# Performance work log

Hardware: AMD Instinct MI355X
Metric: run time of the kernel (lower is better)

## Reference

```python
import jax, jax.numpy as jnp
import numpy as np

B, N, P, K, D = 8, 2048, 64, 32, 384
DEPTH, DI, DS, DCONV, DTR, NC = 12, 768, 16, 4, 24, 40
BN_EPS = 1e-5


def _spread_bits(v):
    v = v & 1023
    v = (v | (v << 16)) & 50331903
    v = (v | (v << 8)) & 50393103
    v = (v | (v << 4)) & 51130563
    v = (v | (v << 2)) & 153391689
    return v


def _zkey(x, y, z):
    return _spread_bits(x) | (_spread_bits(y) << 1) | (_spread_bits(z) << 2)


def _sfc_order(xyz, trans):
    lo = xyz.min(0, keepdims=True)
    hi = xyz.max(0, keepdims=True)
    q = jnp.clip(((xyz - lo) / (hi - lo + 1e-6) * 1023.0).astype(jnp.int32), 0, 1023)
    if trans:
        keys = _zkey(q[:, 2], q[:, 1], q[:, 0])
    else:
        keys = _zkey(q[:, 0], q[:, 1], q[:, 2])
    return jnp.argsort(keys)


def _ln(x, g, b):
    m = x.mean(-1, keepdims=True)
    v = jnp.var(x, axis=-1, keepdims=True)
    return (x - m) / jnp.sqrt(v + 1e-5) * g + b


def _bn_eval(x, g, b):
    # BatchNorm in eval mode, running_mean=0 / running_var=1
    return x * (g / np.float32(np.sqrt(1.0 + BN_EPS))) + b


def _patch_embed_one(xyz, w1, b1, g1, be1, w2, b2, g2, be2, w3, b3, g3, be3):
    # xyz: (N,3)
    cidx = (jnp.arange(P) * (N / P)).astype(jnp.int32)
    centers = xyz[cidx]                                      # (P,3)
    d2 = ((centers[:, None, :] - xyz[None, :, :]) ** 2).sum(-1)  # (P,N)
    _, knn = jax.lax.top_k(-d2, K)                           # (P,K) smallest dists
    nx = xyz[knn] - centers[:, None, :]                      # (P,K,3)
    h = jax.nn.gelu(_bn_eval(nx @ w1.T + b1, g1, be1), approximate=False)   # (P,K,64)
    h = jax.nn.gelu(_bn_eval(h @ w2.T + b2, g2, be2), approximate=False)    # (P,K,128)
    h = _bn_eval(h @ w3.T + b3, g3, be3)                     # (P,K,384)
    return h.max(1), centers


def _mamba(x, in_w, conv_w, conv_b, xp_w, dt_w, dt_b, Alog, Dp, out_w):
    # x: (B,L,D)
    Bsz, L, _ = x.shape
    xz = x @ in_w.T                                          # (B,L,2*DI)
    xc, z = xz[..., :DI], xz[..., DI:]
    xpad = jnp.pad(xc, ((0, 0), (DCONV - 1, 0), (0, 0)))
    xc = sum(xpad[:, j:j + L, :] * conv_w[:, j] for j in range(DCONV)) + conv_b
    xc = jax.nn.silu(xc)
    x_dbl = xc @ xp_w.T                                      # (B,L,DTR+2*DS)
    dt = x_dbl[..., :DTR]
    Bm = x_dbl[..., DTR:DTR + DS]
    Cm = x_dbl[..., DTR + DS:]
    delta = jax.nn.softplus(dt @ dt_w.T + dt_b)              # (B,L,DI)
    A = -jnp.exp(Alog)                                       # (DI,DS)

    def step(h, inp):
        d_t, B_t, C_t, u_t = inp                             # (B,DI),(B,DS),(B,DS),(B,DI)
        h = h * jnp.exp(d_t[..., None] * A) + (d_t * u_t)[..., None] * B_t[:, None, :]
        return h, jnp.einsum('bds,bs->bd', h, C_t)

    h0 = jnp.zeros((Bsz, DI, DS), x.dtype)
    inps = (delta.transpose(1, 0, 2), Bm.transpose(1, 0, 2),
            Cm.transpose(1, 0, 2), xc.transpose(1, 0, 2))
    _, ys = jax.lax.scan(step, h0, inps)                     # (L,B,DI)
    y = ys.transpose(1, 0, 2) + Dp * xc
    y = y * jax.nn.silu(z)
    return y @ out_w.T


def setup_inputs() -> dict:
    key = jax.random.key(0)
    ks = iter(jax.random.split(key, 64))
    nrm = lambda *s: jax.random.normal(next(ks), s, jnp.float32) * 0.02
    inp = {
        'data': jax.random.normal(next(ks), (B, N, 3), jnp.float32),
        'pe_w1': nrm(64, 3), 'pe_b1': jnp.zeros(64), 'pe_g1': jnp.ones(64), 'pe_be1': jnp.zeros(64),
        'pe_w2': nrm(128, 64), 'pe_b2': jnp.zeros(128), 'pe_g2': jnp.ones(128), 'pe_be2': jnp.zeros(128),
        'pe_w3': nrm(D, 128), 'pe_b3': jnp.zeros(D), 'pe_g3': jnp.ones(D), 'pe_be3': jnp.zeros(D),
        'oi_h_scale': jnp.ones(D), 'oi_h_shift': jnp.zeros(D),
        'oi_th_scale': jnp.ones(D), 'oi_th_shift': jnp.zeros(D),
        'pos_embed': nrm(1, P, D),
        'blk_ln_g': jnp.ones((DEPTH, D)), 'blk_ln_b': jnp.zeros((DEPTH, D)),
        'blk_in_w': nrm(DEPTH, 2 * DI, D),
        'blk_conv_w': nrm(DEPTH, DI, DCONV), 'blk_conv_b': jnp.zeros((DEPTH, DI)),
        'blk_xp_w': nrm(DEPTH, DTR + 2 * DS, DI),
        'blk_dt_w': nrm(DEPTH, DI, DTR), 'blk_dt_b': jnp.full((DEPTH, DI), -4.0),
        'blk_Alog': jnp.tile(jnp.log(jnp.arange(1, DS + 1, dtype=jnp.float32)), (DEPTH, DI, 1)),
        'blk_D': jnp.ones((DEPTH, DI)),
        'blk_out_w': nrm(DEPTH, D, DI),
        'norm_g': jnp.ones(D), 'norm_b': jnp.zeros(D),
        'mlp_w1': nrm(256, D), 'mlp_b1': jnp.zeros(256),
        'mlp_w2': nrm(64, 256), 'mlp_b2': jnp.zeros(64),
        'mlp_w3': nrm(NC, 64), 'mlp_b3': jnp.zeros(NC),
    }
    return inp


def reference(data, pe_w1, pe_b1, pe_g1, pe_be1, pe_w2, pe_b2, pe_g2, pe_be2,
              pe_w3, pe_b3, pe_g3, pe_be3, oi_h_scale, oi_h_shift, oi_th_scale,
              oi_th_shift, pos_embed, blk_ln_g, blk_ln_b, blk_in_w, blk_conv_w,
              blk_conv_b, blk_xp_w, blk_dt_w, blk_dt_b, blk_Alog, blk_D,
              blk_out_w, norm_g, norm_b, mlp_w1, mlp_b1, mlp_w2, mlp_b2,
              mlp_w3, mlp_b3):
    xyz = data[:, :, :3]
    tokens, centers = jax.vmap(
        _patch_embed_one, in_axes=(0,) + (None,) * 12)(
        xyz, pe_w1, pe_b1, pe_g1, pe_be1, pe_w2, pe_b2, pe_g2, pe_be2,
        pe_w3, pe_b3, pe_g3, pe_be3)                         # (B,P,D),(B,P,3)
    order_h = jax.vmap(lambda c: _sfc_order(c, False))(centers)
    order_th = jax.vmap(lambda c: _sfc_order(c, True))(centers)
    th = jnp.take_along_axis(tokens, order_h[:, :, None], axis=1) * oi_h_scale + oi_h_shift
    tth = jnp.take_along_axis(tokens, order_th[:, :, None], axis=1) * oi_th_scale + oi_th_shift
    t = jnp.concatenate([th + pos_embed, tth + pos_embed], axis=1)  # (B,2P,D)
    for i in range(DEPTH):
        t = t + _mamba(_ln(t, blk_ln_g[i], blk_ln_b[i]),
                       blk_in_w[i], blk_conv_w[i], blk_conv_b[i], blk_xp_w[i],
                       blk_dt_w[i], blk_dt_b[i], blk_Alog[i], blk_D[i], blk_out_w[i])
    t = _ln(t, norm_g, norm_b)
    x = t.mean(1)
    x = jax.nn.relu(x @ mlp_w1.T + mlp_b1)
    x = jax.nn.relu(x @ mlp_w2.T + mlp_b2)
    return x @ mlp_w3.T + mlp_b3
```

## Files before the change

kernel.cpp:

```cpp
#include <hip/hip_runtime.h>
#include <math.h>

#define BB 8
#define NN 2048
#define PP 64
#define KK 32
#define DD 384
#define DEPTH 12
#define DI 768
#define DS 16
#define DCONV 4
#define DTR 24
#define NC 40
#define LL 128
#define XROW (DTR + 2 * DS)
#define NR (BB * LL)
#define XZSPLIT 12
#define OSPLIT 4

using bf16x8 = __attribute__((ext_vector_type(8))) short;
using floatx4 = __attribute__((ext_vector_type(4))) float;

__device__ __forceinline__ float gelu_exact(float x) {
    return 0.5f * x * (1.0f + erff(x * 0.70710678118654752440f));
}
__device__ __forceinline__ float siluf(float x) {
    return x / (1.0f + expf(-x));
}
__device__ __forceinline__ unsigned short f2bf(float f) {
    unsigned u = __float_as_uint(f);
    u += 0x7fffu + ((u >> 16) & 1u);
    return (unsigned short)(u >> 16);
}
__device__ __forceinline__ float bf2f(short s) {
    return __uint_as_float(((unsigned)(unsigned short)s) << 16);
}
__device__ __forceinline__ unsigned spread_bits(unsigned v) {
    v &= 1023u;
    v = (v | (v << 16)) & 50331903u;
    v = (v | (v << 8)) & 50393103u;
    v = (v | (v << 4)) & 51130563u;
    v = (v | (v << 2)) & 153391689u;
    return v;
}

__global__ void k_w2bf(const float* __restrict__ src, unsigned short* __restrict__ dst, int n)
{
    int i = (blockIdx.x * 256 + threadIdx.x) * 4;
    if (i >= n) return;
    float4 v = *(const float4*)(src + i);
    dst[i + 0] = f2bf(v.x);
    dst[i + 1] = f2bf(v.y);
    dst[i + 2] = f2bf(v.z);
    dst[i + 3] = f2bf(v.w);
}

__global__ void k_xp2bf(const float* __restrict__ xp, unsigned short* __restrict__ dst)
{
    int idx = blockIdx.x * 256 + threadIdx.x;
    if (idx >= DEPTH * 64 * DI) return;
    int i = idx / (64 * DI);
    int rem = idx - i * 64 * DI;
    int n = rem / DI, k = rem % DI;
    float v = (n < XROW) ? xp[(size_t)i * XROW * DI + (size_t)n * DI + k] : 0.f;
    dst[idx] = f2bf(v);
}

__global__ __launch_bounds__(256) void k_knn(const float* __restrict__ data,
                                             int* __restrict__ knn_out,
                                             float* __restrict__ centers)
{
    const int bp = blockIdx.x;
    const int b = bp >> 6, p = bp & 63;
    const int tid = threadIdx.x;
    const int lane = tid & 63, wid = tid >> 6;
    const float* X = data + (size_t)b * NN * 3;

    const float cx = X[p * 32 * 3 + 0];
    const float cy = X[p * 32 * 3 + 1];
    const float cz = X[p * 32 * 3 + 2];
    if (tid == 0) {
        centers[(b * PP + p) * 3 + 0] = cx;
        centers[(b * PP + p) * 3 + 1] = cy;
        centers[(b * PP + p) * 3 + 2] = cz;
    }

    unsigned long long pk[8];
#pragma unroll
    for (int q = 0; q < 8; q++) {
        int i = tid + 256 * q;
        float dx = cx - X[i * 3 + 0];
        float dy = cy - X[i * 3 + 1];
        float dz = cz - X[i * 3 + 2];
        float d2 = dx * dx + dy * dy + dz * dz;
        pk[q] = ((unsigned long long)__float_as_uint(d2) << 32) | (unsigned)i;
    }

    __shared__ unsigned long long wred[4];
    __shared__ int klist[KK];
    for (int k = 0; k < KK; k++) {
        unsigned long long m = pk[0];
#pragma unroll
        for (int q = 1; q < 8; q++) m = pk[q] < m ? pk[q] : m;
#pragma unroll
        for (int off = 32; off; off >>= 1) {
            unsigned long long o = __shfl_xor(m, off);
            m = o < m ? o : m;
        }
        if (lane == 0) wred[wid] = m;
        __syncthreads();
        unsigned long long g = wred[0];
#pragma unroll
        for (int w = 1; w < 4; w++) g = wred[w] < g ? wred[w] : g;
#pragma unroll
        for (int q = 0; q < 8; q++)
            if (pk[q] == g) pk[q] = ~0ull;
        if (tid == 0) klist[k] = (int)(g & 0xffffffffu);
        __syncthreads();
    }
    if (tid < KK) knn_out[bp * KK + tid] = klist[tid];
}

__global__ __launch_bounds__(256) void k_pe_mlp(
    const float* __restrict__ data, const int* __restrict__ knn_in,
    const float* __restrict__ w1, const float* __restrict__ b1,
    const float* __restrict__ g1, const float* __restrict__ be1,
    const float* __restrict__ w2, const float* __restrict__ b2,
    const float* __restrict__ g2, const float* __restrict__ be2,
    const unsigned short* __restrict__ w3bf, const float* __restrict__ b3,
    const float* __restrict__ g3, const float* __restrict__ be3,
    float* __restrict__ tokens)
{
    const int bp = blockIdx.x;
    const int b = bp >> 6, p = bp & 63;
    const int tid = threadIdx.x;
    const float* X = data + (size_t)b * NN * 3;
    const float inv_den = 0.99999500003749968752f;

    __shared__ float nxs[KK * 3];
    __shared__ float h1s[KK * 64];
    __shared__ short h2b[KK * 136];

    const float cx = X[p * 32 * 3 + 0];
    const float cy = X[p * 32 * 3 + 1];
    const float cz = X[p * 32 * 3 + 2];
    if (tid < KK) {
        int q = knn_in[bp * KK + tid];
        nxs[tid * 3 + 0] = X[q * 3 + 0] - cx;
        nxs[tid * 3 + 1] = X[q * 3 + 1] - cy;
        nxs[tid * 3 + 2] = X[q * 3 + 2] - cz;
    }
    __syncthreads();

    for (int e = tid; e < KK * 64; e += 256) {
        int j = e >> 6, c = e & 63;
        float v = nxs[j * 3 + 0] * w1[c * 3 + 0] + nxs[j * 3 + 1] * w1[c * 3 + 1] +
                  nxs[j * 3 + 2] * w1[c * 3 + 2] + b1[c];
        v = v * (g1[c] * inv_den) + be1[c];
        h1s[j * 64 + c] = gelu_exact(v);
    }
    __syncthreads();

    for (int e = tid; e < KK * 128; e += 256) {
        int j = e >> 7, c = e & 127;
        const float4* wr = (const float4*)(w2 + (size_t)c * 64);
        const float4* hr = (const float4*)(h1s + j * 64);
        float acc = 0.f;
#pragma unroll
        for (int q = 0; q < 16; q++) {
            float4 wv = wr[q], hv = hr[q];
            acc += hv.x * wv.x + hv.y * wv.y + hv.z * wv.z + hv.w * wv.w;
        }
        float v = (acc + b2[c]) * (g2[c] * inv_den) + be2[c];
        h2b[j * 136 + c] = (short)f2bf(gelu_exact(v));
    }
    __syncthreads();

    const int wave = tid >> 6, lane = tid & 63;
    const int quad = lane >> 4, r = lane & 15;
    floatx4 acc3[2][6] = {};
#pragma unroll
    for (int ks = 0; ks < 4; ks++) {
        const int k0 = ks * 32;
        bf16x8 af[2];
        af[0] = *(const bf16x8*)(h2b + (size_t)r * 136 + quad * 8 + k0);
        af[1] = *(const bf16x8*)(h2b + (size_t)(16 + r) * 136 + quad * 8 + k0);
        bf16x8 bfv[6];
#pragma unroll
        for (int nj = 0; nj < 6; nj++) {
            int n = wave * 96 + nj * 16 + r;
            bfv[nj] = *(const bf16x8*)(w3bf + (size_t)n * 128 + quad * 8 + k0);
        }
#pragma unroll
        for (int mi = 0; mi < 2; mi++)
#pragma unroll
            for (int nj = 0; nj < 6; nj++)
                acc3[mi][nj] = __builtin_amdgcn_mfma_f32_16x16x32_bf16(af[mi], bfv[nj], acc3[mi][nj], 0, 0, 0);
    }
#pragma unroll
    for (int nj = 0; nj < 6; nj++) {
        int col = wave * 96 + nj * 16 + r;
        float sc = g3[col] * inv_den;
        float offc = b3[col] * sc + be3[col];
        float m = -3.4e38f;
#pragma unroll
        for (int mi = 0; mi < 2; mi++)
#pragma unroll
            for (int r2 = 0; r2 < 4; r2++)
                m = fmaxf(m, acc3[mi][nj][r2] * sc + offc);
        m = fmaxf(m, __shfl_xor(m, 16));
        m = fmaxf(m, __shfl_xor(m, 32));
        if (quad == 0) tokens[(size_t)bp * DD + col] = m;
    }
}

__global__ __launch_bounds__(64) void k_sfc(const float* __restrict__ centers,
                                            int* __restrict__ order_h,
                                            int* __restrict__ order_th)
{
    const int b = blockIdx.x;
    const int tid = threadIdx.x;
    float cc[3];
    cc[0] = centers[(b * PP + tid) * 3 + 0];
    cc[1] = centers[(b * PP + tid) * 3 + 1];
    cc[2] = centers[(b * PP + tid) * 3 + 2];

    __shared__ float csh[PP][3];
    __shared__ float slo[3], shi[3];
    csh[tid][0] = cc[0]; csh[tid][1] = cc[1]; csh[tid][2] = cc[2];
    __syncthreads();
    if (tid == 0) {
        for (int k = 0; k < 3; k++) {
            float lo = csh[0][k], hi = csh[0][k];
            for (int j = 1; j < PP; j++) { lo = fminf(lo, csh[j][k]); hi = fmaxf(hi, csh[j][k]); }
            slo[k] = lo; shi[k] = hi;
        }
    }
    __syncthreads();

    int q[3];
    for (int k = 0; k < 3; k++) {
        float t = (cc[k] - slo[k]) / (shi[k] - slo[k] + 1e-6f) * 1023.0f;
        int qi = (int)t;
        qi = qi < 0 ? 0 : (qi > 1023 ? 1023 : qi);
        q[k] = qi;
    }
    unsigned kh = spread_bits((unsigned)q[0]) | (spread_bits((unsigned)q[1]) << 1) |
                  (spread_bits((unsigned)q[2]) << 2);
    unsigned kt = spread_bits((unsigned)q[2]) | (spread_bits((unsigned)q[1]) << 1) |
                  (spread_bits((unsigned)q[0]) << 2);

    __shared__ unsigned khs[PP], kts[PP];
    khs[tid] = kh; kts[tid] = kt;
    __syncthreads();
    int rh = 0, rt = 0;
    for (int j = 0; j < PP; j++) {
        unsigned a = khs[j];
        rh += (a < kh) || (a == kh && j < tid);
        unsigned c = kts[j];
        rt += (c < kt) || (c == kt && j < tid);
    }
    order_h[b * PP + rh] = tid;
    order_th[b * PP + rt] = tid;
}

__global__ void k_build_t(const float* __restrict__ tokens,
                          const int* __restrict__ order_h, const int* __restrict__ order_th,
                          const float* __restrict__ hs, const float* __restrict__ hb,
                          const float* __restrict__ ts, const float* __restrict__ tb,
                          const float* __restrict__ pos, float* __restrict__ t)
{
    int idx = blockIdx.x * blockDim.x + threadIdx.x;
    if (idx >= BB * LL * DD) return;
    int d = idx % DD;
    int l = (idx / DD) % LL;
    int b = idx / (DD * LL);
    float v;
    if (l < PP) {
        int src = order_h[b * PP + l];
        v = tokens[((size_t)b * PP + src) * DD + d] * hs[d] + hb[d] + pos[l * DD + d];
    } else {
        int ll2 = l - PP;
        int src = order_th[b * PP + ll2];
        v = tokens[((size_t)b * PP + src) * DD + d] * ts[d] + tb[d] + pos[ll2 * DD + d];
    }
    t[idx] = v;
}

__global__ __launch_bounds__(256) void k_stats(float* __restrict__ t,
                                               const float* __restrict__ parts,
                                               const float* __restrict__ g,
                                               const float* __restrict__ gb,
                                               unsigned short* __restrict__ tbf)
{
    const int tid = threadIdx.x;
    const int wid = tid >> 6, lane = tid & 63;
    const int row = blockIdx.x * 4 + wid;
    const size_t base = (size_t)row * DD;
    float v[6];
    float s = 0.f;
#pragma unroll
    for (int j = 0; j < 6; j++) {
        int i = lane + 64 * j;
        float x = t[base + i];
        if (parts) {
            x += parts[base + i] + parts[(size_t)NR * DD + base + i] +
                 parts[2 * (size_t)NR * DD + base + i] + parts[3 * (size_t)NR * DD + base + i];
            t[base + i] = x;
        }
        v[j] = x; s += x;
    }
#pragma unroll
    for (int off = 32; off; off >>= 1) s += __shfl_xor(s, off);
    float mean = s * (1.0f / DD);
    float vs = 0.f;
#pragma unroll
    for (int j = 0; j < 6; j++) { float dd = v[j] - mean; vs += dd * dd; }
#pragma unroll
    for (int off = 32; off; off >>= 1) vs += __shfl_xor(vs, off);
    float inv = 1.0f / sqrtf(vs * (1.0f / DD) + 1e-5f);
#pragma unroll
    for (int j = 0; j < 6; j++) {
        int i = lane + 64 * j;
        tbf[base + i] = f2bf((v[j] - mean) * inv * g[i] + gb[i]);
    }
}

__global__ __launch_bounds__(256) void k_mfma_xz(
    const unsigned short* __restrict__ tbf,
    const unsigned short* __restrict__ inwbf,
    const float* __restrict__ cw, const float* __restrict__ cb,
    unsigned short* __restrict__ xcbf, unsigned short* __restrict__ zsbf)
{
    __shared__ short ct[128][136];
    const int tid = threadIdx.x;
    const int wave = tid >> 6, lane = tid & 63;
    const int quad = lane >> 4, r = lane & 15;
    const int wm = wave >> 1, wn = wave & 1;
    const int b = blockIdx.y;
    const int n0 = blockIdx.x * 128;
    const int m0 = b * 128 + wm * 64;

    floatx4 acc[4][4] = {};
    const unsigned short* Ab = tbf + (size_t)(m0 + r) * DD + quad * 8;
    const unsigned short* Bb = inwbf + (size_t)(n0 + wn * 64 + r) * DD + quad * 8;
    for (int k0 = 0; k0 < DD; k0 += 32) {
        bf16x8 af[4], bfv[4];
#pragma unroll
        for (int i = 0; i < 4; i++) {
            af[i] = *(const bf16x8*)(Ab + (size_t)(i * 16) * DD + k0);
            bfv[i] = *(const bf16x8*)(Bb + (size_t)(i * 16) * DD + k0);
        }
#pragma unroll
        for (int i = 0; i < 4; i++)
#pragma unroll
            for (int j = 0; j < 4; j++)
                acc[i][j] = __builtin_amdgcn_mfma_f32_16x16x32_bf16(af[i], bfv[j], acc[i][j], 0, 0, 0);
    }

#pragma unroll
    for (int i = 0; i < 4; i++)
#pragma unroll
        for (int r2 = 0; r2 < 4; r2++) {
            short* cp = &ct[wm * 64 + i * 16 + quad * 4 + r2][wn * 64 + r];
#pragma unroll
            for (int j = 0; j < 4; j++)
                cp[j * 16] = (short)f2bf(acc[i][j][r2]);
        }
    __syncthreads();

    const int l0 = (tid >> 4) * 8;
    const int c0 = (tid & 15) * 8;
    if (n0 < DI) {
        float cwv[8][4], cbv[8];
#pragma unroll
        for (int q = 0; q < 8; q++) {
            *(float4*)cwv[q] = *(const float4*)(cw + (size_t)(n0 + c0 + q) * 4);
            cbv[q] = cb[n0 + c0 + q];
        }
#pragma unroll
        for (int dl = 0; dl < 8; dl++) {
            const int l = l0 + dl;
            float u[8];
#pragma unroll
            for (int q = 0; q < 8; q++) u[q] = cbv[q];
#pragma unroll
            for (int j = 0; j < DCONV; j++) {
                int lt = l - (DCONV - 1) + j;
                if (lt >= 0) {
                    bf16x8 x = *(const bf16x8*)&ct[lt][c0];
#pragma unroll
                    for (int q = 0; q < 8; q++) u[q] += bf2f(x[q]) * cwv[q][j];
                }
            }
            unsigned short o[8];
#pragma unroll
            for (int q = 0; q < 8; q++) o[q] = f2bf(siluf(u[q]));
            *(bf16x8*)(xcbf + (size_t)(b * LL + l) * DI + n0 + c0) = *(bf16x8*)o;
        }
    } else {
        const int nz = n0 - DI;
#pragma unroll
        for (int dl = 0; dl < 8; dl++) {
            const int l = l0 + dl;
            bf16x8 x = *(const bf16x8*)&ct[l][c0];
            unsigned short o[8];
#pragma unroll
            for (int q = 0; q < 8; q++) o[q] = f2bf(siluf(bf2f(x[q])));
            *(bf16x8*)(zsbf + (size_t)(b * LL + l) * DI + nz + c0) = *(bf16x8*)o;
        }
    }
}

__global__ __launch_bounds__(256) void k_mfma_xdbl(
    const unsigned short* __restrict__ xcbf,
    const unsigned short* __restrict__ xpbf,
    float* __restrict__ parts)
{
    const int tid = threadIdx.x;
    const int wave = tid >> 6, lane = tid & 63;
    const int quad = lane >> 4, r = lane & 15;
    const int rowbase = blockIdx.y * 256 + wave * 64;
    const int z = blockIdx.z;
    const int kbeg = z * (DI / XZSPLIT);

    floatx4 acc[4][4] = {};
#pragma unroll
    for (int k0 = 0; k0 < DI / XZSPLIT; k0 += 32) {
        bf16x8 af[4], bfv[4];
#pragma unroll
        for (int i = 0; i < 4; i++) {
            af[i] = *(const bf16x8*)(xcbf + (size_t)(rowbase + i * 16 + r) * DI + kbeg + k0 + quad * 8);
            bfv[i] = *(const bf16x8*)(xpbf + (size_t)(i * 16 + r) * DI + kbeg + k0 + quad * 8);
        }
#pragma unroll
        for (int mi = 0; mi < 4; mi++)
#pragma unroll
            for (int nj = 0; nj < 4; nj++)
                acc[mi][nj] = __builtin_amdgcn_mfma_f32_16x16x32_bf16(af[mi], bfv[nj], acc[mi][nj], 0, 0, 0);
    }

    float* out = parts + (size_t)z * NR * XROW;
#pragma unroll
    for (int mi = 0; mi < 4; mi++)
#pragma unroll
        for (int nj = 0; nj < 4; nj++) {
            int col = nj * 16 + r;
            if (col < XROW) {
#pragma unroll
                for (int r2 = 0; r2 < 4; r2++) {
                    int row = rowbase + mi * 16 + quad * 4 + r2;
                    out[(size_t)row * XROW + col] = acc[mi][nj][r2];
                }
            }
        }
}

__global__ void k_xred(const float* __restrict__ parts, float* __restrict__ xdbl)
{
    int i = blockIdx.x * 256 + threadIdx.x;
    if (i >= NR * XROW) return;
    float s = 0.f;
#pragma unroll
    for (int z = 0; z < XZSPLIT; z++) s += parts[(size_t)z * NR * XROW + i];
    xdbl[i] = s;
}

__global__ __launch_bounds__(256) void k_scan(
    const float* __restrict__ xdbl,
    const unsigned short* __restrict__ xcbf, const unsigned short* __restrict__ zsbf,
    const float* __restrict__ dtw, const float* __restrict__ dtb,
    const float* __restrict__ Alog, const float* __restrict__ Dp,
    unsigned short* __restrict__ ybf)
{
    const int tid = threadIdx.x;
    const int b = blockIdx.x / (DI / 2);
    const int d0 = (blockIdx.x % (DI / 2)) * 2;

    __shared__ float da[LL][33];
    __shared__ float Bsh[LL][DS];
    __shared__ float Csh[LL][DS];
    __shared__ float dus[LL][2];
    __shared__ float us[LL][2];
    __shared__ float zs[LL][2];
    __shared__ float ApL[2][DS][9];
    __shared__ float HlL[2][DS][9];
    __shared__ float hst[2][DS][9];

    {
        const int t = tid >> 1, dl = tid & 1;
        const int d = d0 + dl;
        const size_t row = (size_t)b * LL + t;
        const float* xd = xdbl + row * XROW;
        const float* w = dtw + d * DTR;
        float acc = dtb[d];
#pragma unroll
        for (int k = 0; k < DTR; k++) acc += xd[k] * w[k];
        float delta = fmaxf(acc, 0.f) + log1pf(__expf(-fabsf(acc)));
        float u = bf2f((short)xcbf[row * DI + d]);
        dus[t][dl] = delta * u;
        us[t][dl] = u;
        zs[t][dl] = bf2f((short)zsbf[row * DI + d]);
#pragma unroll
        for (int s = 0; s < DS; s++)
            da[t][2 * s + dl] = __expf(delta * (-__expf(Alog[d * DS + s])));
    }
    for (int i = tid; i < LL * DS; i += 256) {
        int t = i >> 4, s = i & 15;
        const float* xd = xdbl + ((size_t)b * LL + t) * XROW;
        Bsh[t][s] = xd[DTR + s];
        Csh[t][s] = xd[DTR + DS + s];
    }
    __syncthreads();

    const int s = tid & 15;
    const int dl = (tid >> 4) & 1;
    const int c = tid >> 5;

    {
        float h = 0.f, Ap = 1.f;
#pragma unroll
        for (int q = 0; q < 16; q++) {
            int t = c * 16 + q;
            float a = da[t][2 * s + dl];
            h = h * a + dus[t][dl] * Bsh[t][s];
            Ap *= a;
        }
        ApL[dl][s][c] = Ap;
        HlL[dl][s][c] = h;
    }
    __syncthreads();
    if (tid < 32) {
        int s2 = tid & 15, d2 = tid >> 4;
        float hs = 0.f;
#pragma unroll
        for (int cc = 0; cc < 8; cc++) {
            hst[d2][s2][cc] = hs;
            hs = ApL[d2][s2][cc] * hs + HlL[d2][s2][cc];
        }
    }
    __syncthreads();

    {
        const float Dd = Dp[d0 + dl];
        float h = hst[dl][s][c];
        unsigned short* yc = ybf + ((size_t)b * LL + c * 16) * DI + (d0 + dl);
#pragma unroll
        for (int q = 0; q < 16; q++) {
            int t = c * 16 + q;
            float a = da[t][2 * s + dl];
            h = h * a + dus[t][dl] * Bsh[t][s];
            float p = h * Csh[t][s];
            p += __shfl_xor(p, 1, 16);
            p += __shfl_xor(p, 2, 16);
            p += __shfl_xor(p, 4, 16);
            p += __shfl_xor(p, 8, 16);
            if (s == 0) yc[(size_t)q * DI] = f2bf((p + Dd * us[t][dl]) * zs[t][dl]);
        }
    }
}

__global__ __launch_bounds__(256) void k_mfma_gemm(
    const unsigned short* __restrict__ Abf, int lda,
    const unsigned short* __restrict__ Wbf, int ldb,
    float* __restrict__ C, int ldc, size_t cstride, int kchunk)
{
    const int tid = threadIdx.x;
    const int wave = tid >> 6, lane = tid & 63;
    const int quad = lane >> 4, r = lane & 15;
    const int wm = wave >> 1, wn = wave & 1;
    const int m0 = blockIdx.y * 128 + wm * 64;
    const int n0 = blockIdx.x * 128 + wn * 64;
    const int kbeg = blockIdx.z * kchunk;
    float* Cz = C + (size_t)blockIdx.z * cstride;

    floatx4 acc[4][4] = {};

    const unsigned short* Ab = Abf + (size_t)(m0 + r) * lda + quad * 8 + kbeg;
    const unsigned short* Bb = Wbf + (size_t)(n0 + r) * ldb + quad * 8 + kbeg;

    for (int k0 = 0; k0 < kchunk; k0 += 32) {
        bf16x8 af[4], bf[4];
#pragma unroll
        for (int i = 0; i < 4; i++) {
            af[i] = *(const bf16x8*)(Ab + (size_t)(i * 16) * lda + k0);
            bf[i] = *(const bf16x8*)(Bb + (size_t)(i * 16) * ldb + k0);
        }
#pragma unroll
        for (int i = 0; i < 4; i++)
#pragma unroll
            for (int j = 0; j < 4; j++)
                acc[i][j] = __builtin_amdgcn_mfma_f32_16x16x32_bf16(af[i], bf[j], acc[i][j], 0, 0, 0);
    }

#pragma unroll
    for (int i = 0; i < 4; i++)
#pragma unroll
        for (int r2 = 0; r2 < 4; r2++) {
            float* cp = Cz + (size_t)(m0 + i * 16 + quad * 4 + r2) * ldc + n0 + r;
#pragma unroll
            for (int j = 0; j < 4; j++)
                cp[j * 16] = acc[i][j][r2];
        }
}

__global__ __launch_bounds__(64) void k_ln(const float* __restrict__ x,
                                           const float* __restrict__ parts,
                                           const float* __restrict__ g,
                                           const float* __restrict__ bb,
                                           float* __restrict__ y)
{
    const int row = blockIdx.x;
    const int tid = threadIdx.x;
    const size_t base = (size_t)row * DD;
    float v[6];
    float s = 0.f;
#pragma unroll
    for (int j = 0; j < 6; j++) {
        int i = tid + 64 * j;
        float xv = x[base + i] + parts[base + i] + parts[(size_t)NR * DD + base + i] +
                   parts[2 * (size_t)NR * DD + base + i] + parts[3 * (size_t)NR * DD + base + i];
        v[j] = xv; s += xv;
    }
#pragma unroll
    for (int off = 32; off; off >>= 1) s += __shfl_xor(s, off);
    float mean = s * (1.0f / DD);
    float vs = 0.f;
#pragma unroll
    for (int j = 0; j < 6; j++) { float dd = v[j] - mean; vs += dd * dd; }
#pragma unroll
    for (int off = 32; off; off >>= 1) vs += __shfl_xor(vs, off);
    float inv = 1.0f / sqrtf(vs * (1.0f / DD) + 1e-5f);
#pragma unroll
    for (int j = 0; j < 6; j++) {
        int i = tid + 64 * j;
        y[base + i] = (v[j] - mean) * inv * g[i] + bb[i];
    }
}

__global__ void k_mean(const float* __restrict__ xln, float* __restrict__ pooled)
{
    int idx = blockIdx.x * blockDim.x + threadIdx.x;
    if (idx >= BB * DD) return;
    int b = idx / DD, d = idx % DD;
    float sv = 0.f;
    for (int l = 0; l < LL; l++) sv += xln[((size_t)b * LL + l) * DD + d];
    pooled[idx] = sv / (float)LL;
}

__global__ __launch_bounds__(256) void k_mlp(const float* __restrict__ pooled,
    const float* __restrict__ w1, const float* __restrict__ b1,
    const float* __restrict__ w2, const float* __restrict__ b2,
    const float* __restrict__ w3, const float* __restrict__ b3,
    float* __restrict__ out)
{
    int b = blockIdx.x, tid = threadIdx.x;
    __shared__ float pl[DD];
    __shared__ float h1[256];
    __shared__ float h2[64];
    for (int i = tid; i < DD; i += 256) pl[i] = pooled[b * DD + i];
    __syncthreads();
    {
        float acc = b1[tid];
        const float* wr = w1 + (size_t)tid * DD;
        for (int k = 0; k < DD; k++) acc += pl[k] * wr[k];
        h1[tid] = fmaxf(acc, 0.f);
    }
    __syncthreads();
    if (tid < 64) {
        float acc = b2[tid];
        const float* wr = w2 + (size_t)tid * 256;
        for (int k = 0; k < 256; k++) acc += h1[k] * wr[k];
        h2[tid] = fmaxf(acc, 0.f);
    }
    __syncthreads();
    if (tid < NC) {
        float acc = b3[tid];
        const float* wr = w3 + (size_t)tid * 64;
        for (int k = 0; k < 64; k++) acc += h2[k] * wr[k];
        out[b * NC + tid] = acc;
    }
}

extern "C" void kernel_launch(void* const* d_in, const int* in_sizes, int n_in,
                              void* d_out, int out_size, void* d_ws, size_t ws_size,
                              hipStream_t stream)
{
    const float* data      = (const float*)d_in[0];
    const float* pe_w1     = (const float*)d_in[1];
    const float* pe_b1     = (const float*)d_in[2];
    const float* pe_g1     = (const float*)d_in[3];
    const float* pe_be1    = (const float*)d_in[4];
    const float* pe_w2     = (const float*)d_in[5];
    const float* pe_b2     = (const float*)d_in[6];
    const float* pe_g2     = (const float*)d_in[7];
    const float* pe_be2    = (const float*)d_in[8];
    const float* pe_w3     = (const float*)d_in[9];
    const float* pe_b3     = (const float*)d_in[10];
    const float* pe_g3     = (const float*)d_in[11];
    const float* pe_be3    = (const float*)d_in[12];
    const float* oi_h_scale  = (const float*)d_in[13];
    const float* oi_h_shift  = (const float*)d_in[14];
    const float* oi_th_scale = (const float*)d_in[15];
    const float* oi_th_shift = (const float*)d_in[16];
    const float* pos_embed = (const float*)d_in[17];
    const float* blk_ln_g  = (const float*)d_in[18];
    const float* blk_ln_b  = (const float*)d_in[19];
    const float* blk_in_w  = (const float*)d_in[20];
    const float* blk_conv_w = (const float*)d_in[21];
    const float* blk_conv_b = (const float*)d_in[22];
    const float* blk_xp_w  = (const float*)d_in[23];
    const float* blk_dt_w  = (const float*)d_in[24];
    const float* blk_dt_b  = (const float*)d_in[25];
    const float* blk_Alog  = (const float*)d_in[26];
    const float* blk_D     = (const float*)d_in[27];
    const float* blk_out_w = (const float*)d_in[28];
    const float* norm_g    = (const float*)d_in[29];
    const float* norm_b    = (const float*)d_in[30];
    const float* mlp_w1    = (const float*)d_in[31];
    const float* mlp_b1    = (const float*)d_in[32];
    const float* mlp_w2    = (const float*)d_in[33];
    const float* mlp_b2    = (const float*)d_in[34];
    const float* mlp_w3    = (const float*)d_in[35];
    const float* mlp_b3    = (const float*)d_in[36];

    float* ws = (float*)d_ws;
    size_t off = 0;
    auto alloc = [&](size_t n) { float* p = ws + off; off += (n + 63) & ~(size_t)63; return p; };
    float* tokens  = alloc((size_t)BB * PP * DD);
    float* centers = alloc((size_t)BB * PP * 3);
    int*   order_h = (int*)alloc((size_t)BB * PP);
    int*   order_th= (int*)alloc((size_t)BB * PP);
    int*   knn_idx = (int*)alloc((size_t)BB * PP * KK);
    float* t    = alloc((size_t)NR * DD);
    float* xln  = alloc((size_t)NR * DD);
    float* xdbl = alloc((size_t)NR * XROW);
    float* pooled = alloc((size_t)BB * DD);
    float* parts_out = alloc((size_t)OSPLIT * NR * DD);
    float* parts_x   = alloc((size_t)XZSPLIT * NR * XROW);
    unsigned short* tbf   = (unsigned short*)alloc((size_t)NR * DD / 2);
    unsigned short* xcbf  = (unsigned short*)alloc((size_t)NR * DI / 2);
    unsigned short* zsbf  = (unsigned short*)alloc((size_t)NR * DI / 2);
    unsigned short* ybf   = (unsigned short*)alloc((size_t)NR * DI / 2);
    unsigned short* inwbf = (unsigned short*)alloc((size_t)DEPTH * 2 * DI * DD / 2);
    unsigned short* owbf  = (unsigned short*)alloc((size_t)DEPTH * DD * DI / 2);
    unsigned short* xpbf  = (unsigned short*)alloc((size_t)DEPTH * 64 * DI / 2);
    unsigned short* w3bf  = (unsigned short*)alloc((size_t)DD * 128 / 2);

    {
        int n1 = DEPTH * 2 * DI * DD;
        int n2 = DEPTH * DD * DI;
        int n3 = DD * 128;
        int n4 = DEPTH * 64 * DI;
        k_w2bf<<<(n1 / 4 + 255) / 256, 256, 0, stream>>>(blk_in_w, inwbf, n1);
        k_w2bf<<<(n2 / 4 + 255) / 256, 256, 0, stream>>>(blk_out_w, owbf, n2);
        k_w2bf<<<(n3 / 4 + 255) / 256, 256, 0, stream>>>(pe_w3, w3bf, n3);
        k_xp2bf<<<(n4 + 255) / 256, 256, 0, stream>>>(blk_xp_w, xpbf);
    }

    k_knn<<<BB * PP, 256, 0, stream>>>(data, knn_idx, centers);
    k_pe_mlp<<<BB * PP, 256, 0, stream>>>(data, knn_idx,
        pe_w1, pe_b1, pe_g1, pe_be1, pe_w2, pe_b2, pe_g2, pe_be2,
        w3bf, pe_b3, pe_g3, pe_be3, tokens);
    k_sfc<<<BB, 64, 0, stream>>>(centers, order_h, order_th);
    {
        int nt = BB * LL * DD;
        k_build_t<<<(nt + 255) / 256, 256, 0, stream>>>(tokens, order_h, order_th,
            oi_h_scale, oi_h_shift, oi_th_scale, oi_th_shift, pos_embed, t);
    }

    for (int i = 0; i < DEPTH; i++) {
        const float* ln_g = blk_ln_g + i * DD;
        const float* ln_b = blk_ln_b + i * DD;
        const float* cw   = blk_conv_w + (size_t)i * DI * DCONV;
        const float* cb   = blk_conv_b + (size_t)i * DI;
        const float* dtw  = blk_dt_w + (size_t)i * DI * DTR;
        const float* dtb  = blk_dt_b + (size_t)i * DI;
        const float* Al   = blk_Alog + (size_t)i * DI * DS;
        const float* Dpp  = blk_D + (size_t)i * DI;
        const unsigned short* inw = inwbf + (size_t)i * 2 * DI * DD;
        const unsigned short* ow  = owbf + (size_t)i * DD * DI;
        const unsigned short* xpb = xpbf + (size_t)i * 64 * DI;

        k_stats<<<NR / 4, 256, 0, stream>>>(t, (i == 0) ? nullptr : parts_out, ln_g, ln_b, tbf);
        k_mfma_xz<<<dim3(12, BB), 256, 0, stream>>>(tbf, inw, cw, cb, xcbf, zsbf);
        k_mfma_xdbl<<<dim3(1, NR / 256, XZSPLIT), 256, 0, stream>>>(xcbf, xpb, parts_x);
        k_xred<<<(NR * XROW + 255) / 256, 256, 0, stream>>>(parts_x, xdbl);
        k_scan<<<BB * DI / 2, 256, 0, stream>>>(xdbl, xcbf, zsbf, dtw, dtb, Al, Dpp, ybf);
        k_mfma_gemm<<<dim3(DD / 128, NR / 128, OSPLIT), 256, 0, stream>>>(
            ybf, DI, ow, DI, parts_out, DD, (size_t)NR * DD, DI / OSPLIT);
    }

    k_ln<<<NR, 64, 0, stream>>>(t, parts_out, norm_g, norm_b, xln);
    k_mean<<<(BB * DD + 255) / 256, 256, 0, stream>>>(xln, pooled);
    k_mlp<<<BB, 256, 0, stream>>>(pooled, mlp_w1, mlp_b1, mlp_w2, mlp_b2, mlp_w3, mlp_b3,
                                  (float*)d_out);
}
```

Baseline: 1.143 ms.

## Fuse x_proj GEMM into in_proj/conv kernel and shrink scan blocks to one channel

The x_proj partial GEMM now runs inside the in_proj+conv kernel. Each of the six xc column tiles multiplies its conv/SiLU output, already in shared memory, by the matching slice of the x_proj weights and writes one partial of six. This removes a separate kernel launch and a reload of xc from global memory, and halves the partial sums that the reduction kernel reads. The scan kernel is also changed from two channels per 256-thread block to one channel per 128-thread block, with B/C loaded per thread, doubling the block count and making the shared-memory indexing simpler. The extra GEMM work falls only on the xc blocks, which are 48 of 96, so the load across blocks becomes uneven.

Measured after the change: 1.158 ms. Within noise of the previous version (+1.3%).

```diff
diff --git a/kernel.cpp b/kernel.cpp
--- a/kernel.cpp
+++ b/kernel.cpp
@@ -15,7 +15,7 @@
 #define LL 128
 #define XROW (DTR + 2 * DS)
 #define NR (BB * LL)
-#define XZSPLIT 12
+#define XPARTS 6
 #define OSPLIT 4
 
 using bf16x8 = __attribute__((ext_vector_type(8))) short;
@@ -330,7 +330,9 @@
     const unsigned short* __restrict__ tbf,
     const unsigned short* __restrict__ inwbf,
     const float* __restrict__ cw, const float* __restrict__ cb,
-    unsigned short* __restrict__ xcbf, unsigned short* __restrict__ zsbf)
+    const unsigned short* __restrict__ xpbf,
+    unsigned short* __restrict__ xcbf, unsigned short* __restrict__ zsbf,
+    float* __restrict__ parts_x)
 {
     __shared__ short ct[128][136];
     const int tid = threadIdx.x;
@@ -378,6 +380,7 @@
             *(float4*)cwv[q] = *(const float4*)(cw + (size_t)(n0 + c0 + q) * 4);
             cbv[q] = cb[n0 + c0 + q];
         }
+        unsigned short ov[8][8];
 #pragma unroll
         for (int dl = 0; dl < 8; dl++) {
             const int l = l0 + dl;
@@ -393,11 +396,49 @@
                     for (int q = 0; q < 8; q++) u[q] += bf2f(x[q]) * cwv[q][j];
                 }
             }
-            unsigned short o[8];
-#pragma unroll
-            for (int q = 0; q < 8; q++) o[q] = f2bf(siluf(u[q]));
-            *(bf16x8*)(xcbf + (size_t)(b * LL + l) * DI + n0 + c0) = *(bf16x8*)o;
-        }
+#pragma unroll
+            for (int q = 0; q < 8; q++) ov[dl][q] = f2bf(siluf(u[q]));
+        }
+        __syncthreads();
+#pragma unroll
+        for (int dl = 0; dl < 8; dl++) {
+            const int l = l0 + dl;
+            *(bf16x8*)&ct[l][c0] = *(bf16x8*)ov[dl];
+            *(bf16x8*)(xcbf + (size_t)(b * LL + l) * DI + n0 + c0) = *(bf16x8*)ov[dl];
+        }
+        __syncthreads();
+
+        const int zi = blockIdx.x;
+        floatx4 acc2[2][4] = {};
+#pragma unroll
+        for (int k0 = 0; k0 < 128; k0 += 32) {
+            bf16x8 af2[2], bfv2[4];
+#pragma unroll
+            for (int i = 0; i < 2; i++)
+                af2[i] = *(const bf16x8*)&ct[wave * 32 + i * 16 + r][k0 + quad * 8];
+#pragma unroll
+            for (int nj = 0; nj < 4; nj++)
+                bfv2[nj] = *(const bf16x8*)(xpbf + (size_t)(nj * 16 + r) * DI + n0 + k0 + quad * 8);
+#pragma unroll
+            for (int i = 0; i < 2; i++)
+#pragma unroll
+                for (int nj = 0; nj < 4; nj++)
+                    acc2[i][nj] = __builtin_amdgcn_mfma_f32_16x16x32_bf16(af2[i], bfv2[nj], acc2[i][nj], 0, 0, 0);
+        }
+        float* out = parts_x + (size_t)zi * NR * XROW;
+#pragma unroll
+        for (int i = 0; i < 2; i++)
+#pragma unroll
+            for (int nj = 0; nj < 4; nj++) {
+                int col = nj * 16 + r;
+                if (col < XROW) {
+#pragma unroll
+                    for (int r2 = 0; r2 < 4; r2++) {
+                        int row = b * LL + wave * 32 + i * 16 + quad * 4 + r2;
+                        out[(size_t)row * XROW + col] = acc2[i][nj][r2];
+                    }
+                }
+            }
     } else {
         const int nz = n0 - DI;
 #pragma unroll
@@ -412,61 +453,17 @@
     }
 }
 
-__global__ __launch_bounds__(256) void k_mfma_xdbl(
-    const unsigned short* __restrict__ xcbf,
-    const unsigned short* __restrict__ xpbf,
-    float* __restrict__ parts)
-{
-    const int tid = threadIdx.x;
-    const int wave = tid >> 6, lane = tid & 63;
-    const int quad = lane >> 4, r = lane & 15;
-    const int rowbase = blockIdx.y * 256 + wave * 64;
-    const int z = blockIdx.z;
-    const int kbeg = z * (DI / XZSPLIT);
-
-    floatx4 acc[4][4] = {};
-#pragma unroll
-    for (int k0 = 0; k0 < DI / XZSPLIT; k0 += 32) {
-        bf16x8 af[4], bfv[4];
-#pragma unroll
-        for (int i = 0; i < 4; i++) {
-            af[i] = *(const bf16x8*)(xcbf + (size_t)(rowbase + i * 16 + r) * DI + kbeg + k0 + quad * 8);
-            bfv[i] = *(const bf16x8*)(xpbf + (size_t)(i * 16 + r) * DI + kbeg + k0 + quad * 8);
-        }
-#pragma unroll
-        for (int mi = 0; mi < 4; mi++)
-#pragma unroll
-            for (int nj = 0; nj < 4; nj++)
-                acc[mi][nj] = __builtin_amdgcn_mfma_f32_16x16x32_bf16(af[mi], bfv[nj], acc[mi][nj], 0, 0, 0);
-    }
-
-    float* out = parts + (size_t)z * NR * XROW;
-#pragma unroll
-    for (int mi = 0; mi < 4; mi++)
-#pragma unroll
-        for (int nj = 0; nj < 4; nj++) {
-            int col = nj * 16 + r;
-            if (col < XROW) {
-#pragma unroll
-                for (int r2 = 0; r2 < 4; r2++) {
-                    int row = rowbase + mi * 16 + quad * 4 + r2;
-                    out[(size_t)row * XROW + col] = acc[mi][nj][r2];
-                }
-            }
-        }
-}
-
 __global__ void k_xred(const float* __restrict__ parts, float* __restrict__ xdbl)
 {
     int i = blockIdx.x * 256 + threadIdx.x;
     if (i >= NR * XROW) return;
     float s = 0.f;
 #pragma unroll
-    for (int z = 0; z < XZSPLIT; z++) s += parts[(size_t)z * NR * XROW + i];
+    for (int z = 0; z < XPARTS; z++) s += parts[(size_t)z * NR * XROW + i];
     xdbl[i] = s;
 }
 
-__global__ __launch_bounds__(256) void k_scan(
+__global__ __launch_bounds__(128) void k_scan(
     const float* __restrict__ xdbl,
     const unsigned short* __restrict__ xcbf, const unsigned short* __restrict__ zsbf,
     const float* __restrict__ dtw, const float* __restrict__ dtb,
@@ -474,22 +471,21 @@
     unsigned short* __restrict__ ybf)
 {
     const int tid = threadIdx.x;
-    const int b = blockIdx.x / (DI / 2);
-    const int d0 = (blockIdx.x % (DI / 2)) * 2;
-
-    __shared__ float da[LL][33];
-    __shared__ float Bsh[LL][DS];
-    __shared__ float Csh[LL][DS];
-    __shared__ float dus[LL][2];
-    __shared__ float us[LL][2];
-    __shared__ float zs[LL][2];
-    __shared__ float ApL[2][DS][9];
-    __shared__ float HlL[2][DS][9];
-    __shared__ float hst[2][DS][9];
+    const int b = blockIdx.x / DI;
+    const int d = blockIdx.x % DI;
+
+    __shared__ float da[LL][17];
+    __shared__ float Bsh[LL][17];
+    __shared__ float Csh[LL][17];
+    __shared__ float dus[LL];
+    __shared__ float us[LL];
+    __shared__ float zs[LL];
+    __shared__ float ApL[DS][9];
+    __shared__ float HlL[DS][9];
+    __shared__ float hst[DS][9];
 
     {
-        const int t = tid >> 1, dl = tid & 1;
-        const int d = d0 + dl;
+        const int t = tid;
         const size_t row = (size_t)b * LL + t;
         const float* xd = xdbl + row * XROW;
         const float* w = dtw + d * DTR;
@@ -498,64 +494,59 @@
         for (int k = 0; k < DTR; k++) acc += xd[k] * w[k];
         float delta = fmaxf(acc, 0.f) + log1pf(__expf(-fabsf(acc)));
         float u = bf2f((short)xcbf[row * DI + d]);
-        dus[t][dl] = delta * u;
-        us[t][dl] = u;
-        zs[t][dl] = bf2f((short)zsbf[row * DI + d]);
-#pragma unroll
-        for (int s = 0; s < DS; s++)
-            da[t][2 * s + dl] = __expf(delta * (-__expf(Alog[d * DS + s])));
-    }
-    for (int i = tid; i < LL * DS; i += 256) {
-        int t = i >> 4, s = i & 15;
-        const float* xd = xdbl + ((size_t)b * LL + t) * XROW;
-        Bsh[t][s] = xd[DTR + s];
-        Csh[t][s] = xd[DTR + DS + s];
+        dus[t] = delta * u;
+        us[t] = u;
+        zs[t] = bf2f((short)zsbf[row * DI + d]);
+#pragma unroll
+        for (int s = 0; s < DS; s++) {
+            da[t][s] = __expf(delta * (-__expf(Alog[d * DS + s])));
+            Bsh[t][s] = xd[DTR + s];
+            Csh[t][s] = xd[DTR + DS + s];
+        }
     }
     __syncthreads();
 
     const int s = tid & 15;
-    const int dl = (tid >> 4) & 1;
-    const int c = tid >> 5;
+    const int c = tid >> 4;
 
     {
         float h = 0.f, Ap = 1.f;
 #pragma unroll
         for (int q = 0; q < 16; q++) {
             int t = c * 16 + q;
-            float a = da[t][2 * s + dl];
-            h = h * a + dus[t][dl] * Bsh[t][s];
+            float a = da[t][s];
+            h = h * a + dus[t] * Bsh[t][s];
             Ap *= a;
         }
-        ApL[dl][s][c] = Ap;
-        HlL[dl][s][c] = h;
-    }
-    __syncthreads();
-    if (tid < 32) {
-        int s2 = tid & 15, d2 = tid >> 4;
+        ApL[s][c] = Ap;
+        HlL[s][c] = h;
+    }
+    __syncthreads();
+    if (tid < DS) {
         float hs = 0.f;
 #pragma unroll
         for (int cc = 0; cc < 8; cc++) {
-            hst[d2][s2][cc] = hs;
-            hs = ApL[d2][s2][cc] * hs + HlL[d2][s2][cc];
+            hst[tid][cc] = hs;
+            hs = ApL[tid][cc] * hs + HlL[tid][cc];
         }
     }
     __syncthreads();
 
     {
-        const float Dd = Dp[d0 + dl];
-        float h = hst[dl][s][c];
-        unsigned short* yc = ybf + ((size_t)b * LL + c * 16) * DI + (d0 + dl);
+        const float Dd = Dp[d];
+        float h = hst[s][c];
+        unsigned short* yc = ybf + ((size_t)b * LL + c * 16) * DI + d;
 #pragma unroll
         for (int q = 0; q < 16; q++) {
             int t = c * 16 + q;
-            float a = da[t][2 * s + dl];
-            h = h * a + dus[t][dl] * Bsh[t][s];
+            float a = da[t][s];
+            h = h * a + dus[t] * Bsh[t][s];
             float p = h * Csh[t][s];
             p += __shfl_xor(p, 1, 16);
             p += __shfl_xor(p, 2, 16);
             p += __shfl_xor(p, 4, 16);
             p += __shfl_xor(p, 8, 16);
-            if (s == 0) yc[(size_t)q * DI] = f2bf((p + Dd * us[t][dl]) * zs[t][dl]);
+            if (s == 0) yc[(size_t)q * DI] = f2bf((p + Dd * us[t]) * zs[t]);
         }
     }
 }
@@ -737,7 +728,7 @@
     float* xdbl = alloc((size_t)NR * XROW);
     float* pooled = alloc((size_t)BB * DD);
     float* parts_out = alloc((size_t)OSPLIT * NR * DD);
-    float* parts_x   = alloc((size_t)XZSPLIT * NR * XROW);
+    float* parts_x   = alloc((size_t)XPARTS * NR * XROW);
     unsigned short* tbf   = (unsigned short*)alloc((size_t)NR * DD / 2);
     unsigned short* xcbf  = (unsigned short*)alloc((size_t)NR * DI / 2);
     unsigned short* zsbf  = (unsigned short*)alloc((size_t)NR * DI / 2);
@@ -783,10 +774,9 @@
         const unsigned short* xpb = xpbf + (size_t)i * 64 * DI;
 
         k_stats<<<NR / 4, 256, 0, stream>>>(t, (i == 0) ? nullptr : parts_out, ln_g, ln_b, tbf);
-        k_mfma_xz<<<dim3(12, BB), 256, 0, stream>>>(tbf, inw, cw, cb, xcbf, zsbf);
-        k_mfma_xdbl<<<dim3(1, NR / 256, XZSPLIT), 256, 0, stream>>>(xcbf, xpb, parts_x);
+        k_mfma_xz<<<dim3(12, BB), 256, 0, stream>>>(tbf, inw, cw, cb, xpb, xcbf, zsbf, parts_x);
         k_xred<<<(NR * XROW + 255) / 256, 256, 0, stream>>>(parts_x, xdbl);
-        k_scan<<<BB * DI / 2, 256, 0, stream>>>(xdbl, xcbf, zsbf, dtw, dtb, Al, Dpp, ybf);
+        k_scan<<<BB * DI, 128, 0, stream>>>(xdbl, xcbf, zsbf, dtw, dtb, Al, Dpp, ybf);
         k_mfma_gemm<<<dim3(DD / 128, NR / 128, OSPLIT), 256, 0, stream>>>(
             ybf, DI, ow, DI, parts_out, DD, (size_t)NR * DD, DI / OSPLIT);
     }
```
